# Performance work log

Measured on AMD Instinct MI355X. Metric: run time of the kernel, lower is better.

## Reference

```python
import jax, jax.numpy as jnp
import numpy as np
import math
from jax import lax

IN_C = 512
OUT_C = 512
K = 3
GROUPS = 1
EXP_NITER = 5
MAXC = max(IN_C, OUT_C)
PAD_A = int(math.ceil((K - 1) / 2))  # left/top pad
PAD_B = int(math.floor((K - 1) / 2))  # right/bottom pad


def pad_fct(x):
    # ConstantPad2d((ceil, floor, ceil, floor), 0) on last two dims
    return jnp.pad(x, ((0, 0), (0, 0), (PAD_A, PAD_B), (PAD_A, PAD_B)))


def fast_matrix_conv(m1, m2, groups=1):
    # m1: (m, n, k1, k2); m2: (nb, m//groups, l1, l2)
    # composes two conv kernels: result (nb, n, k+l-1, k+l-1)
    m, n, k1, k2 = m1.shape
    nb, mb, l1, l2 = m2.shape
    x = jnp.transpose(m1, (1, 0, 2, 3))          # (n, m, k1, k2) -> batch=n, chan=m
    w = jnp.flip(m2, (-2, -1))                   # true convolution via flip
    r = lax.conv_general_dilated(
        x, w, window_strides=(1, 1),
        padding=[(l1 - 1, l1 - 1), (l2 - 1, l2 - 1)],
        dimension_numbers=("NCHW", "OIHW", "NCHW"),
        feature_group_count=groups,
    )                                            # (n, nb, k1+l1-1, k2+l2-1)
    return jnp.transpose(r, (1, 0, 2, 3))


def identity_kernel():
    gic = MAXC // GROUPS
    eye = jnp.eye(gic, dtype=jnp.float32)[:, :, None, None]     # (gic, gic, 1, 1)
    eye = jnp.tile(eye[None], (GROUPS, 1, 1, 1, 1)).reshape(MAXC, gic, 1, 1)
    return pad_fct(eye)                                          # (MAXC, gic, K, K)


def setup_inputs() -> dict:
    key = jax.random.key(0)
    kernel = jax.random.normal(key, (MAXC, MAXC // GROUPS, K, K), dtype=jnp.float32) * 0.05
    return {"kernel": kernel}


def reference(kernel):
    kg = kernel + identity_kernel()
    ki = kernel
    for i in range(2, EXP_NITER + 1):
        ki = fast_matrix_conv(ki, kernel, GROUPS) / float(i)
        kg = pad_fct(kg) + ki
    g = GROUPS
    kh, kw = kg.shape[-2], kg.shape[-1]
    kg = kg.reshape(g, MAXC // g, MAXC // g, kh, kw)
    kg = kg[:, : OUT_C // g, : IN_C // g, :, :]
    return kg.reshape(OUT_C, IN_C // g, kh, kw)
```

## Files before the change

### kernel.cpp

```cpp
#include <hip/hip_runtime.h>
#include <stdint.h>

#define C 512
#define C2 262144

typedef __attribute__((ext_vector_type(8))) short bf16x8;
typedef __attribute__((ext_vector_type(4))) float f32x4;

__device__ __forceinline__ unsigned short f2bf(float f) {
    union { float f; uint32_t u; } v; v.f = f;
    uint32_t u = v.u;
    u += 0x7fffu + ((u >> 16) & 1u);
    return (unsigned short)(u >> 16);
}
__device__ __forceinline__ float bf2f(unsigned short h) {
    union { uint32_t u; float f; } v; v.u = ((uint32_t)h) << 16;
    return v.f;
}

#define GL2LDS16(g, l) __builtin_amdgcn_global_load_lds( \
    (const __attribute__((address_space(1))) void*)(g),  \
    (__attribute__((address_space(3))) void*)(l), 16, 0, 0)

__device__ __forceinline__ bf16x8 ldsr16(const char* p) {
    bf16x8 r;
    asm volatile("ds_read_b128 %0, %1"
                 : "=v"(r)
                 : "v"((__attribute__((address_space(3))) const void*)p));
    return r;
}

__device__ __forceinline__ int nth_valid(int mask, int n) {
    int pq = 0;
    while (true) {
        if (mask & 1) { if (n == 0) return pq; --n; }
        mask >>= 1; ++pq;
    }
}

__global__ void k_transform(const float* __restrict__ K,
                            unsigned short* __restrict__ Kt,
                            unsigned short* __restrict__ KtT,
                            float* __restrict__ Ktf) {
    int t = blockIdx.x * 256 + threadIdx.x;
    int a = t >> 9, b = t & 511;
#pragma unroll
    for (int j = 0; j < 9; ++j) {
        float v = K[(size_t)t * 9 + j];
        unsigned short h = f2bf(v);
        Kt[(size_t)j * C2 + t] = h;
        KtT[(size_t)j * C2 + (size_t)b * C + a] = h;
        Ktf[(size_t)j * C2 + (size_t)b * C + a] = v;
    }
}

__global__ void k_sched(int* __restrict__ sched, int split_mask) {
    __shared__ int hist[4][10];
    __shared__ int base[4][10];
    const int tid = threadIdx.x;
    if (tid < 40) ((int*)hist)[tid] = 0;
    if (tid < 4) sched[tid] = 0;
    __syncthreads();
    const int offs[5] = {0, 25, 74, 155, 276};
    const int Loff[4] = {0, 120, 400, 904};
    int step = -1, yx = 0, cW = 0, cD = 0;
    if (tid < 276) {
#pragma unroll
        for (int s = 0; s < 4; ++s)
            if (tid >= offs[s] && tid < offs[s + 1]) { step = s; yx = tid - offs[s]; }
        const int s_out = 5 + 2 * step, s_in = s_out - 2;
        const int y = yx / s_out, x = yx % s_out;
        int vy = 0, vx = 0;
#pragma unroll
        for (int p = 0; p < 3; ++p) {
            if (y - p >= 0 && y - p < s_in) ++vy;
            if (x - p >= 0 && x - p < s_in) ++vx;
        }
        const int V = vy * vx;
        const bool sp = ((split_mask >> step) & 1) && (V >= 6);
        cW = sp ? (V + 1) / 2 : V;
        cD = V - cW;
        atomicAdd(&hist[step][cW], 1);
        if (cD > 0) atomicAdd(&hist[step][cD], 1);
    }
    __syncthreads();
    if (tid < 4) {
        int a = 0;
        for (int v = 9; v >= 1; --v) { base[tid][v] = a; a += hist[tid][v]; hist[tid][v] = 0; }
    }
    __syncthreads();
    if (tid < 276) {
        int* L = sched + 4 + Loff[step];
        {
            const int idx = atomicAdd(&hist[step][cW], 1);
            int* w = L + (base[step][cW] + idx) * 4;
            w[0] = yx * 8 + 0; w[1] = yx * 8 + 2; w[2] = yx * 8 + 4; w[3] = yx * 8 + 6;
        }
        if (cD > 0) {
            const int idx = atomicAdd(&hist[step][cD], 1);
            int* d = L + (base[step][cD] + idx) * 4;
            d[0] = yx * 8 + 1; d[1] = yx * 8 + 3; d[2] = yx * 8 + 5; d[3] = yx * 8 + 7;
        }
    }
}

__global__ __launch_bounds__(256) void k_merge(
    unsigned short* __restrict__ Out, const unsigned short* __restrict__ P,
    const int* __restrict__ list)
{
    const int code = list[blockIdx.x];
    if (!(code & 1)) return;
    const int quad = (code >> 1) & 3, yx = code >> 3;
    const int i0 = (quad & 1) * 256, o0 = (quad >> 1) * 256;
    const int t = threadIdx.x;
    const int r = blockIdx.y * 16 + (t >> 4);
    const int c = (t & 15) * 16;
    const size_t base = ((size_t)yx * C + i0 + r) * C + o0 + c;
    bf16x8* po = (bf16x8*)(Out + base);
    const bf16x8* pp = (const bf16x8*)(P + base);
    bf16x8 a0 = po[0], a1 = po[1];
    bf16x8 b0 = pp[0], b1 = pp[1];
#pragma unroll
    for (int k = 0; k < 8; ++k) {
        a0[k] = (short)f2bf(bf2f((unsigned short)a0[k]) + bf2f((unsigned short)b0[k]));
        a1[k] = (short)f2bf(bf2f((unsigned short)a1[k]) + bf2f((unsigned short)b1[k]));
    }
    po[0] = a0; po[1] = a1;
}

__global__ __launch_bounds__(512, 2) void k_gemm(
    const unsigned short* __restrict__ A,
    const unsigned short* __restrict__ Bm,
    unsigned short* __restrict__ Out,
    int s_in, int s_out, float alpha,
    int* __restrict__ ctr, const int* __restrict__ list, int n_items,
    unsigned short* __restrict__ Pout, int split)
{
    __shared__ __align__(16) char lds[131072];
    __shared__ int s_item;

    const int tid = threadIdx.x;
    const int lane = tid & 63, wid = tid >> 6;
    const int wr = wid >> 2, wc = wid & 3;
    const int l15 = lane & 15, lhi = lane >> 4;

    const int soff = (tid >> 3) * 1024 + ((((tid & 7) ^ ((tid >> 3) & 7))) << 4);
    const int t16 = tid * 16;

    const int coff0 = ((lhi ^ (l15 & 7)) << 4);
    const int coff1 = (((4 + lhi) ^ (l15 & 7)) << 4);
    const int aoff = wr * 16384 + l15 * 128;
    const int boff = 32768 + wc * 8192 + l15 * 128;

    const char* Abase = (const char*)A;
    const char* Bbase = (const char*)Bm;

#define STAGE4(SRC, DSTOFF) { \
        const char* s_ = (SRC) + soff; \
        GL2LDS16(s_,          lds + (DSTOFF) + t16); \
        GL2LDS16(s_ + 65536,  lds + (DSTOFF) + 8192 + t16); \
        GL2LDS16(s_ + 131072, lds + (DSTOFF) + 16384 + t16); \
        GL2LDS16(s_ + 196608, lds + (DSTOFF) + 24576 + t16); \
    }

    for (;;) {
        __syncthreads();
        if (tid == 0) s_item = atomicAdd(ctr, 1);
        __syncthreads();
        const int itm = s_item;
        if (itm >= n_items) break;
        const int code = list[itm];
        const int isD = code & 1;
        const int quad = (code >> 1) & 3;
        const int yx = code >> 3;
        const int i0 = (quad & 1) * 256, o0 = (quad >> 1) * 256;
        const int y = yx / s_out, x = yx % s_out;

        int mask = 0, V = 0;
        for (int pq = 0; pq < 9; ++pq) {
            int u = y - pq / 3, v = x - pq % 3;
            if (u >= 0 && u < s_in && v >= 0 && v < s_in) { mask |= 1 << pq; ++V; }
        }
        const int h = (split && V >= 6) ? (V + 1) / 2 : V;
        const int c0 = isD ? h : 0;
        const int cnt = isD ? (V - h) : h;
        unsigned short* ob = isD ? Pout : Out;

        auto slabA = [&](int pq) {
            int u = y - pq / 3, v = x - pq % 3;
            return Abase + ((size_t)(u * s_in + v) * C + i0) * (size_t)(C * 2);
        };
        auto slabB = [&](int pq) {
            return Bbase + ((size_t)pq * C + o0) * (size_t)(C * 2);
        };
        const int pq0 = nth_valid(mask, c0);
        const char* slA = slabA(pq0);
        const char* slB = slabB(pq0);
        const char* nsA = slA;
        const char* nsB = slB;
        if (cnt > 1) { int p1 = nth_valid(mask, c0 + 1); nsA = slabA(p1); nsB = slabB(p1); }

        f32x4 acc[8][4] = {};
        bf16x8 bBa[4], bBb[4];
        bf16x8 aE[4], aO[4];

        STAGE4(slA, 0)
        STAGE4(slB, 32768)
        asm volatile("s_waitcnt vmcnt(0)" ::: "memory");
        __builtin_amdgcn_s_barrier();
        __builtin_amdgcn_sched_barrier(0);
#pragma unroll
        for (int n = 0; n < 4; ++n)
            bBa[n] = ldsr16(lds + boff + n * 2048 + coff0);
#pragma unroll
        for (int mi = 0; mi < 4; ++mi)
            aE[mi] = ldsr16(lds + aoff + mi * 2048 + coff0);

        const int NI = 8 * cnt;
        for (int it = 0; it < NI; ++it) {
            const int itl = it & 7;
            const bool lastq = (itl == 7);
            const bool dummy = lastq && (((it >> 3) + 1) >= cnt);
            const char* sAe = lastq ? nsA : slA;
            const char* sBe = lastq ? nsB : slB;
            const int kb = lastq ? 0 : (itl + 1) * 128;
            const char* cur = lds + (it & 1) * 65536;
            const char* nxt = lds + ((it & 1) ^ 1) * 65536;

#define PHASE(PH) { \
        constexpr int mh_ = (PH) & 1; \
        constexpr int mhn_ = ((PH) + 1) & 1; \
        constexpr int parn_ = ((PH) == 3) ? 0 : (((PH) + 1) >> 1); \
        const int coffn_ = parn_ ? coff1 : coff0; \
         \
        { \
            const char* ab_ = ((PH) == 3) ? nxt : cur; \
            _Pragma("unroll") for (int mi = 0; mi < 4; ++mi) { \
                bf16x8 t0 = ldsr16(ab_ + aoff + mhn_ * 8192 + mi * 2048 + coffn_); \
                if constexpr (((PH) & 1) == 0) aO[mi] = t0; else aE[mi] = t0; \
            } \
        } \
         \
        if constexpr ((PH) == 1) { \
            _Pragma("unroll") for (int n = 0; n < 4; ++n) \
                bBb[n] = ldsr16(cur + boff + n * 2048 + coff1); \
        } \
        if constexpr ((PH) == 3) { \
            _Pragma("unroll") for (int n = 0; n < 4; ++n) \
                bBa[n] = ldsr16(nxt + boff + n * 2048 + coff0); \
        } \
         \
        if constexpr ((PH) == 0) { if (!dummy) STAGE4(sAe + kb, ((it & 1) ^ 1) * 65536) } \
        if constexpr ((PH) == 1) { if (!dummy) STAGE4(sBe + kb, ((it & 1) ^ 1) * 65536 + 32768) } \
        if constexpr ((PH) == 1 || (PH) == 3) { \
            asm volatile("s_waitcnt lgkmcnt(8)" ::: "memory"); \
        } else { \
            asm volatile("s_waitcnt lgkmcnt(4)" ::: "memory"); \
        } \
        __builtin_amdgcn_sched_barrier(0); \
        __builtin_amdgcn_s_setprio(1); \
        _Pragma("unroll") for (int mi = 0; mi < 4; ++mi) \
        _Pragma("unroll") for (int n = 0; n < 4; ++n) { \
            if constexpr ((PH) == 0) \
                acc[mi][n] = __builtin_amdgcn_mfma_f32_16x16x32_bf16(aE[mi], bBa[n], acc[mi][n], 0, 0, 0); \
            else if constexpr ((PH) == 1) \
                acc[4 + mi][n] = __builtin_amdgcn_mfma_f32_16x16x32_bf16(aO[mi], bBa[n], acc[4 + mi][n], 0, 0, 0); \
            else if constexpr ((PH) == 2) \
                acc[mi][n] = __builtin_amdgcn_mfma_f32_16x16x32_bf16(aE[mi], bBb[n], acc[mi][n], 0, 0, 0); \
            else \
                acc[4 + mi][n] = __builtin_amdgcn_mfma_f32_16x16x32_bf16(aO[mi], bBb[n], acc[4 + mi][n], 0, 0, 0); \
        } \
        __builtin_amdgcn_s_setprio(0); \
        if constexpr ((PH) == 2) { \
            asm volatile("s_waitcnt vmcnt(0)" ::: "memory"); \
            __builtin_amdgcn_s_barrier(); \
            __builtin_amdgcn_sched_barrier(0); \
        } \
        if constexpr ((PH) == 3) { \
            __builtin_amdgcn_s_barrier(); \
            __builtin_amdgcn_sched_barrier(0); \
        } \
    }

            PHASE(0) PHASE(1) PHASE(2) PHASE(3)
#undef PHASE

            if (lastq) {
                slA = nsA; slB = nsB;
                int vn = (it >> 3) + 2;
                if (vn < cnt) {
                    int pqn = nth_valid(mask, c0 + vn);
                    nsA = slabA(pqn); nsB = slabB(pqn);
                }
            }
        }
        asm volatile("s_waitcnt lgkmcnt(0)" ::: "memory");
        __builtin_amdgcn_sched_barrier(0);

#pragma unroll
        for (int M = 0; M < 8; ++M) {
#pragma unroll
            for (int r = 0; r < 4; ++r) {
                const int irow = i0 + wr * 128 + M * 16 + lhi * 4 + r;
                unsigned short* op = ob + ((size_t)yx * C + irow) * C
                                   + o0 + wc * 64 + l15;
#pragma unroll
                for (int n = 0; n < 4; ++n)
                    op[n * 16] = f2bf(acc[M][n][r] * alpha);
            }
        }
    }
#undef STAGE4
    asm volatile("s_waitcnt vmcnt(0)" ::: "memory");
}

__global__ __launch_bounds__(256) void k_final(
    const unsigned short* __restrict__ Ka, int sa, int ofa,
    const unsigned short* __restrict__ Kb, int sb, int ofb,
    const float* __restrict__ Ktf, float* __restrict__ kg, int init)
{
    __shared__ float L[64 * 121];
    const int i = blockIdx.x;
    const int o0 = blockIdx.y * 64;
    const int tid = threadIdx.x, lane = tid & 63, wid = tid >> 6;

    for (int idx = tid; idx < 64 * 121; idx += 256) L[idx] = 0.f;
    __syncthreads();

    const int sa2 = sa * sa;
    for (int yxv = wid; yxv < sa2; yxv += 4) {
        float v = bf2f(Ka[((size_t)yxv * C + i) * C + o0 + lane]);
        int yy = yxv / sa + ofa, xx = yxv % sa + ofa;
        L[lane * 121 + yy * 11 + xx] += v;
    }
    __syncthreads();
    const int sb2 = sb * sb;
    for (int yxv = wid; yxv < sb2; yxv += 4) {
        float v = bf2f(Kb[((size_t)yxv * C + i) * C + o0 + lane]);
        int yy = yxv / sb + ofb, xx = yxv % sb + ofb;
        L[lane * 121 + yy * 11 + xx] += v;
    }
    __syncthreads();
    if (init) {
        for (int j = wid; j < 9; j += 4) {
            float v = Ktf[(size_t)j * C2 + (size_t)i * C + o0 + lane];
            if (j == 4 && (o0 + lane) == i) v += 1.0f;
            L[lane * 121 + (j / 3 + 4) * 11 + (j % 3 + 4)] += v;
        }
    }
    __syncthreads();
    if (init) {
        for (int idx = tid; idx < 64 * 121; idx += 256) {
            int ol = idx / 121, w = idx - ol * 121;
            kg[((size_t)(o0 + ol) * C + i) * 121 + w] = L[idx];
        }
    } else {
        for (int idx = tid; idx < 64 * 121; idx += 256) {
            int ol = idx / 121, w = idx - ol * 121;
            kg[((size_t)(o0 + ol) * C + i) * 121 + w] += L[idx];
        }
    }
}

__global__ __launch_bounds__(256) void k_final4(
    const unsigned short* __restrict__ K2, const unsigned short* __restrict__ K3,
    const unsigned short* __restrict__ K4, const unsigned short* __restrict__ K5,
    const float* __restrict__ Ktf, float* __restrict__ kg)
{
    __shared__ float L[64 * 121];
    const int i = blockIdx.x;
    const int o0 = blockIdx.y * 64;
    const int tid = threadIdx.x, lane = tid & 63, wid = tid >> 6;

    for (int idx = tid; idx < 64 * 121; idx += 256) L[idx] = 0.f;
    __syncthreads();

#define ADDSRC(SRC, S, OFS) { \
        const int s2_ = (S) * (S); \
        for (int yxv = wid; yxv < s2_; yxv += 4) { \
            float v = bf2f((SRC)[((size_t)yxv * C + i) * C + o0 + lane]); \
            int yy = yxv / (S) + (OFS), xx = yxv % (S) + (OFS); \
            L[lane * 121 + yy * 11 + xx] += v; \
        } \
        __syncthreads(); \
    }
    ADDSRC(K2, 5, 3) ADDSRC(K3, 7, 2) ADDSRC(K4, 9, 1) ADDSRC(K5, 11, 0)
#undef ADDSRC

    for (int j = wid; j < 9; j += 4) {
        float v = Ktf[(size_t)j * C2 + (size_t)i * C + o0 + lane];
        if (j == 4 && (o0 + lane) == i) v += 1.0f;
        L[lane * 121 + (j / 3 + 4) * 11 + (j % 3 + 4)] += v;
    }
    __syncthreads();
    for (int idx = tid; idx < 64 * 121; idx += 256) {
        int ol = idx / 121, w = idx - ol * 121;
        kg[((size_t)(o0 + ol) * C + i) * 121 + w] = L[idx];
    }
}

extern "C" void kernel_launch(void* const* d_in, const int* in_sizes, int n_in,
                              void* d_out, int out_size, void* d_ws, size_t ws_size,
                              hipStream_t stream) {
    const float* K = (const float*)d_in[0];
    float* kg = (float*)d_out;
    char* ws = (char*)d_ws;

    unsigned short* Kt  = (unsigned short*)(ws);
    unsigned short* KtT = (unsigned short*)(ws + (size_t)4718592);
    float*          Ktf = (float*)         (ws + (size_t)9437184);

    const bool big = (ws_size >= (size_t)163585616);

    if (big) {
        unsigned short* Ki2 = (unsigned short*)(ws + (size_t)18874368);
        unsigned short* Ki3 = (unsigned short*)(ws + (size_t)31981568);
        unsigned short* Ki4 = (unsigned short*)(ws + (size_t)57671680);
        unsigned short* Ki5 = (unsigned short*)(ws + (size_t)100139008);
        int* sch = (int*)(ws + (size_t)163577856);
        int* lst = sch + 4;
        unsigned short* Pb = Ki5;

        k_transform<<<1024, 256, 0, stream>>>(K, Kt, KtT, Ktf);
        k_sched<<<1, 320, 0, stream>>>(sch, 0x7);
        k_gemm<<<256, 512, 0, stream>>>(KtT, Kt, Ki2, 3, 5, 0.5f,
                                        sch + 0, lst + 0, 120, Pb, 1);
        k_merge<<<dim3(120, 16), 256, 0, stream>>>(Ki2, Pb, lst + 0);
        k_gemm<<<256, 512, 0, stream>>>(Ki2, Kt, Ki3, 5, 7, 1.0f / 3.0f,
                                        sch + 1, lst + 120, 280, Pb, 1);
        k_merge<<<dim3(280, 16), 256, 0, stream>>>(Ki3, Pb, lst + 120);
        k_gemm<<<256, 512, 0, stream>>>(Ki3, Kt, Ki4, 7, 9, 0.25f,
                                        sch + 2, lst + 400, 504, Pb, 1);
        k_merge<<<dim3(504, 16), 256, 0, stream>>>(Ki4, Pb, lst + 400);
        k_gemm<<<256, 512, 0, stream>>>(Ki4, Kt, Ki5, 9, 11, 0.2f,
                                        sch + 3, lst + 904, 484, Pb, 0);
        k_final4<<<dim3(512, 8), 256, 0, stream>>>(Ki2, Ki3, Ki4, Ki5, Ktf, kg);
    } else {
        unsigned short* P1 = (unsigned short*)(ws + (size_t)18874368);
        unsigned short* P2 = (unsigned short*)(ws + (size_t)61341696);
        int* sch = (int*)(ws + (size_t)124780544);
        int* lst = sch + 4;
        unsigned short* Pb2 = P2;
        unsigned short* Pb3 = P1 + 6553600;

        k_transform<<<1024, 256, 0, stream>>>(K, Kt, KtT, Ktf);
        k_sched<<<1, 320, 0, stream>>>(sch, 0x3);
        k_gemm<<<256, 512, 0, stream>>>(KtT, Kt, P1, 3, 5, 0.5f,
                                        sch + 0, lst + 0, 120, Pb2, 1);
        k_merge<<<dim3(120, 16), 256, 0, stream>>>(P1, Pb2, lst + 0);
        k_gemm<<<256, 512, 0, stream>>>(P1, Kt, P2, 5, 7, 1.0f / 3.0f,
                                        sch + 1, lst + 120, 280, Pb3, 1);
        k_merge<<<dim3(280, 16), 256, 0, stream>>>(P2, Pb3, lst + 120);
        k_final<<<dim3(512, 8), 256, 0, stream>>>(P1, 5, 3, P2, 7, 2, Ktf, kg, 1);
        k_gemm<<<256, 512, 0, stream>>>(P2, Kt, P1, 7, 9, 0.25f,
                                        sch + 2, lst + 400, 324, Pb2, 0);
        k_gemm<<<256, 512, 0, stream>>>(P1, Kt, P2, 9, 11, 0.2f,
                                        sch + 3, lst + 904, 484, Pb2, 0);
        k_final<<<dim3(512, 8), 256, 0, stream>>>(P1, 9, 1, P2, 11, 0, Ktf, kg, 0);
    }
}
```

Before: 544.6 us.

## Generalize split-K scheduling to three chunks and vectorize final accumulation loads

```diff
diff --git a/kernel.cpp b/kernel.cpp
--- a/kernel.cpp
+++ b/kernel.cpp
@@ -54,7 +54,7 @@
     }
 }
 
-__global__ void k_sched(int* __restrict__ sched, int split_mask) {
+__global__ void k_sched(int* __restrict__ sched, int splits) {
     __shared__ int hist[4][10];
     __shared__ int base[4][10];
     const int tid = threadIdx.x;
@@ -62,8 +62,8 @@
     if (tid < 4) sched[tid] = 0;
     __syncthreads();
     const int offs[5] = {0, 25, 74, 155, 276};
-    const int Loff[4] = {0, 120, 400, 904};
-    int step = -1, yx = 0, cW = 0, cD = 0;
+    const int Loff[4] = {0, 140, 504, 1008};
+    int step = -1, yx = 0, V = 0, nch = 1, bsz = 0, rem = 0;
     if (tid < 276) {
 #pragma unroll
         for (int s = 0; s < 4; ++s)
@@ -76,12 +76,12 @@
             if (y - p >= 0 && y - p < s_in) ++vy;
             if (x - p >= 0 && x - p < s_in) ++vx;
         }
-        const int V = vy * vx;
-        const bool sp = ((split_mask >> step) & 1) && (V >= 6);
-        cW = sp ? (V + 1) / 2 : V;
-        cD = V - cW;
-        atomicAdd(&hist[step][cW], 1);
-        if (cD > 0) atomicAdd(&hist[step][cD], 1);
+        V = vy * vx;
+        const int sp = (splits >> (4 * step)) & 15;
+        nch = (V >= 6 && sp > 1) ? sp : 1;
+        bsz = V / nch; rem = V % nch;
+        for (int j = 0; j < nch; ++j)
+            atomicAdd(&hist[step][bsz + (j < rem ? 1 : 0)], 1);
     }
     __syncthreads();
     if (tid < 4) {
@@ -91,41 +91,48 @@
     __syncthreads();
     if (tid < 276) {
         int* L = sched + 4 + Loff[step];
-        {
-            const int idx = atomicAdd(&hist[step][cW], 1);
-            int* w = L + (base[step][cW] + idx) * 4;
-            w[0] = yx * 8 + 0; w[1] = yx * 8 + 2; w[2] = yx * 8 + 4; w[3] = yx * 8 + 6;
-        }
-        if (cD > 0) {
-            const int idx = atomicAdd(&hist[step][cD], 1);
-            int* d = L + (base[step][cD] + idx) * 4;
-            d[0] = yx * 8 + 1; d[1] = yx * 8 + 3; d[2] = yx * 8 + 5; d[3] = yx * 8 + 7;
+        for (int j = 0; j < nch; ++j) {
+            const int sz = bsz + (j < rem ? 1 : 0);
+            const int idx = atomicAdd(&hist[step][sz], 1);
+            int* w = L + (base[step][sz] + idx) * 4;
+            w[0] = yx * 16 + 0 + j; w[1] = yx * 16 + 4 + j;
+            w[2] = yx * 16 + 8 + j; w[3] = yx * 16 + 12 + j;
         }
     }
 }
 
 __global__ __launch_bounds__(256) void k_merge(
-    unsigned short* __restrict__ Out, const unsigned short* __restrict__ P,
-    const int* __restrict__ list)
+    unsigned short* __restrict__ Out, const unsigned short* __restrict__ P1,
+    const unsigned short* __restrict__ P2, const int* __restrict__ list,
+    int has3)
 {
     const int code = list[blockIdx.x];
-    if (!(code & 1)) return;
-    const int quad = (code >> 1) & 3, yx = code >> 3;
+    if ((code & 3) != 1) return;
+    const int quad = (code >> 2) & 3, yx = code >> 4;
     const int i0 = (quad & 1) * 256, o0 = (quad >> 1) * 256;
     const int t = threadIdx.x;
     const int r = blockIdx.y * 16 + (t >> 4);
     const int c = (t & 15) * 16;
     const size_t base = ((size_t)yx * C + i0 + r) * C + o0 + c;
     bf16x8* po = (bf16x8*)(Out + base);
-    const bf16x8* pp = (const bf16x8*)(P + base);
-    bf16x8 a0 = po[0], a1 = po[1];
-    bf16x8 b0 = pp[0], b1 = pp[1];
-#pragma unroll
-    for (int k = 0; k < 8; ++k) {
-        a0[k] = (short)f2bf(bf2f((unsigned short)a0[k]) + bf2f((unsigned short)b0[k]));
-        a1[k] = (short)f2bf(bf2f((unsigned short)a1[k]) + bf2f((unsigned short)b1[k]));
-    }
-    po[0] = a0; po[1] = a1;
+    const bf16x8* p1 = (const bf16x8*)(P1 + base);
+    const bf16x8* p2 = (const bf16x8*)(P2 + base);
+#pragma unroll
+    for (int h = 0; h < 2; ++h) {
+        bf16x8 a = po[h], b = p1[h];
+#pragma unroll
+        for (int k = 0; k < 8; ++k) {
+            float s = bf2f((unsigned short)a[k]) + bf2f((unsigned short)b[k]);
+            a[k] = (short)f2bf(s);
+        }
+        if (has3) {
+            bf16x8 cvec = p2[h];
+#pragma unroll
+            for (int k = 0; k < 8; ++k)
+                a[k] = (short)f2bf(bf2f((unsigned short)a[k]) + bf2f((unsigned short)cvec[k]));
+        }
+        po[h] = a;
+    }
 }
 
 __global__ __launch_bounds__(512, 2) void k_gemm(
@@ -134,7 +141,8 @@
     unsigned short* __restrict__ Out,
     int s_in, int s_out, float alpha,
     int* __restrict__ ctr, const int* __restrict__ list, int n_items,
-    unsigned short* __restrict__ Pout, int split)
+    unsigned short* __restrict__ Pb1, unsigned short* __restrict__ Pb2,
+    int split)
 {
     __shared__ __align__(16) char lds[131072];
     __shared__ int s_item;
@@ -170,9 +178,9 @@
         const int itm = s_item;
         if (itm >= n_items) break;
         const int code = list[itm];
-        const int isD = code & 1;
-        const int quad = (code >> 1) & 3;
-        const int yx = code >> 3;
+        const int j = code & 3;
+        const int quad = (code >> 2) & 3;
+        const int yx = code >> 4;
         const int i0 = (quad & 1) * 256, o0 = (quad >> 1) * 256;
         const int y = yx / s_out, x = yx % s_out;
 
@@ -181,10 +189,11 @@
             int u = y - pq / 3, v = x - pq % 3;
             if (u >= 0 && u < s_in && v >= 0 && v < s_in) { mask |= 1 << pq; ++V; }
         }
-        const int h = (split && V >= 6) ? (V + 1) / 2 : V;
-        const int c0 = isD ? h : 0;
-        const int cnt = isD ? (V - h) : h;
-        unsigned short* ob = isD ? Pout : Out;
+        const int nch = (split > 1 && V >= 6) ? split : 1;
+        const int bsz = V / nch, rem = V % nch;
+        const int cnt = bsz + (j < rem ? 1 : 0);
+        const int c0 = j * bsz + (j < rem ? j : rem);
+        unsigned short* ob = (j == 0) ? Out : ((j == 1) ? Pb1 : Pb2);
 
         auto slabA = [&](int pq) {
             int u = y - pq / 3, v = x - pq % 3;
@@ -376,11 +385,13 @@
     __syncthreads();
 
 #define ADDSRC(SRC, S, OFS) { \
-        const int s2_ = (S) * (S); \
-        for (int yxv = wid; yxv < s2_; yxv += 4) { \
-            float v = bf2f((SRC)[((size_t)yxv * C + i) * C + o0 + lane]); \
-            int yy = yxv / (S) + (OFS), xx = yxv % (S) + (OFS); \
-            L[lane * 121 + yy * 11 + xx] += v; \
+        const int total_ = (S) * (S) * 8; \
+        for (int idx = tid; idx < total_; idx += 256) { \
+            const int yxv = idx >> 3, l3 = idx & 7; \
+            bf16x8 v = *(const bf16x8*)&(SRC)[((size_t)yxv * C + i) * C + o0 + l3 * 8]; \
+            const int w = (yxv / (S) + (OFS)) * 11 + yxv % (S) + (OFS); \
+            _Pragma("unroll") for (int k = 0; k < 8; ++k) \
+                L[(l3 * 8 + k) * 121 + w] += bf2f((unsigned short)v[k]); \
         } \
         __syncthreads(); \
     }
@@ -419,21 +430,22 @@
         unsigned short* Ki5 = (unsigned short*)(ws + (size_t)100139008);
         int* sch = (int*)(ws + (size_t)163577856);
         int* lst = sch + 4;
-        unsigned short* Pb = Ki5;
+        unsigned short* PbA = Ki5;
+        unsigned short* PbB = Ki4;
 
         k_transform<<<1024, 256, 0, stream>>>(K, Kt, KtT, Ktf);
-        k_sched<<<1, 320, 0, stream>>>(sch, 0x7);
+        k_sched<<<1, 320, 0, stream>>>(sch, 0x1233);
         k_gemm<<<256, 512, 0, stream>>>(KtT, Kt, Ki2, 3, 5, 0.5f,
-                                        sch + 0, lst + 0, 120, Pb, 1);
-        k_merge<<<dim3(120, 16), 256, 0, stream>>>(Ki2, Pb, lst + 0);
+                                        sch + 0, lst + 0, 140, PbA, PbB, 3);
+        k_merge<<<dim3(140, 16), 256, 0, stream>>>(Ki2, PbA, PbB, lst + 0, 1);
         k_gemm<<<256, 512, 0, stream>>>(Ki2, Kt, Ki3, 5, 7, 1.0f / 3.0f,
-                                        sch + 1, lst + 120, 280, Pb, 1);
-        k_merge<<<dim3(280, 16), 256, 0, stream>>>(Ki3, Pb, lst + 120);
+                                        sch + 1, lst + 140, 364, PbA, PbB, 3);
+        k_merge<<<dim3(364, 16), 256, 0, stream>>>(Ki3, PbA, PbB, lst + 140, 1);
         k_gemm<<<256, 512, 0, stream>>>(Ki3, Kt, Ki4, 7, 9, 0.25f,
-                                        sch + 2, lst + 400, 504, Pb, 1);
-        k_merge<<<dim3(504, 16), 256, 0, stream>>>(Ki4, Pb, lst + 400);
+                                        sch + 2, lst + 504, 504, PbA, PbA, 2);
+        k_merge<<<dim3(504, 16), 256, 0, stream>>>(Ki4, PbA, PbA, lst + 504, 0);
         k_gemm<<<256, 512, 0, stream>>>(Ki4, Kt, Ki5, 9, 11, 0.2f,
-                                        sch + 3, lst + 904, 484, Pb, 0);
+                                        sch + 3, lst + 1008, 484, PbA, PbA, 1);
         k_final4<<<dim3(512, 8), 256, 0, stream>>>(Ki2, Ki3, Ki4, Ki5, Ktf, kg);
     } else {
         unsigned short* P1 = (unsigned short*)(ws + (size_t)18874368);
@@ -444,18 +456,18 @@
         unsigned short* Pb3 = P1 + 6553600;
 
         k_transform<<<1024, 256, 0, stream>>>(K, Kt, KtT, Ktf);
-        k_sched<<<1, 320, 0, stream>>>(sch, 0x3);
+        k_sched<<<1, 320, 0, stream>>>(sch, 0x1122);
         k_gemm<<<256, 512, 0, stream>>>(KtT, Kt, P1, 3, 5, 0.5f,
-                                        sch + 0, lst + 0, 120, Pb2, 1);
-        k_merge<<<dim3(120, 16), 256, 0, stream>>>(P1, Pb2, lst + 0);
+                                        sch + 0, lst + 0, 140, Pb2, Pb2, 2);
+        k_merge<<<dim3(140, 16), 256, 0, stream>>>(P1, Pb2, Pb2, lst + 0, 0);
         k_gemm<<<256, 512, 0, stream>>>(P1, Kt, P2, 5, 7, 1.0f / 3.0f,
-                                        sch + 1, lst + 120, 280, Pb3, 1);
-        k_merge<<<dim3(280, 16), 256, 0, stream>>>(P2, Pb3, lst + 120);
+                                        sch + 1, lst + 140, 364, Pb3, Pb3, 2);
+        k_merge<<<dim3(364, 16), 256, 0, stream>>>(P2, Pb3, Pb3, lst + 140, 0);
         k_final<<<dim3(512, 8), 256, 0, stream>>>(P1, 5, 3, P2, 7, 2, Ktf, kg, 1);
         k_gemm<<<256, 512, 0, stream>>>(P2, Kt, P1, 7, 9, 0.25f,
-                                        sch + 2, lst + 400, 324, Pb2, 0);
+                                        sch + 2, lst + 504, 324, Pb2, Pb2, 1);
         k_gemm<<<256, 512, 0, stream>>>(P1, Kt, P2, 9, 11, 0.2f,
-                                        sch + 3, lst + 904, 484, Pb2, 0);
+                                        sch + 3, lst + 1008, 484, Pb2, Pb2, 1);
         k_final<<<dim3(512, 8), 256, 0, stream>>>(P1, 9, 1, P2, 11, 0, Ktf, kg, 0);
     }
 }
```

Result: faster. 515.1 us (median of 2 runs) (-5.4%).
